# Optimization experiments

Measured on AMD Instinct MI355X. Metric: run time of the kernel, lower is better.

## Reference

```python
import jax, jax.numpy as jnp
import numpy as np
from jax import lax

B, S, D, H = 256, 1024, 64, 128


def setup_inputs() -> dict:
    key = jax.random.key(0)
    ks = jax.random.split(key, 11)
    s_in = 1.0 / np.sqrt(H)  # torch RNNCell/Linear init scale (uniform bound); normal scale ok for testing
    return {
        "inputs": jax.random.normal(ks[0], (B, S, D), jnp.float32),
        "Wih_fw": jax.random.normal(ks[1], (H, D), jnp.float32) * s_in,
        "Whh_fw": jax.random.normal(ks[2], (H, H), jnp.float32) * s_in,
        "bih_fw": jax.random.normal(ks[3], (H,), jnp.float32) * s_in,
        "bhh_fw": jax.random.normal(ks[4], (H,), jnp.float32) * s_in,
        "Wih_bw": jax.random.normal(ks[5], (H, D), jnp.float32) * s_in,
        "Whh_bw": jax.random.normal(ks[6], (H, H), jnp.float32) * s_in,
        "bih_bw": jax.random.normal(ks[7], (H,), jnp.float32) * s_in,
        "bhh_bw": jax.random.normal(ks[8], (H,), jnp.float32) * s_in,
        "fc_W": jax.random.normal(ks[9], (1, 2 * H), jnp.float32) * (1.0 / np.sqrt(2 * H)),
        "fc_b": jnp.zeros((1,), jnp.float32),
    }


def _run_dir(inputs, Wih, Whh, bih, bhh, reverse):
    # Precompute input projection for all timesteps: [B,S,H]
    xp = jnp.einsum('bsd,hd->bsh', inputs, Wih) + bih + bhh
    WhhT = Whh.T

    def step(h, x_t):  # x_t: [B,H]
        h_new = jnp.tanh(x_t + h @ WhhT)
        return h_new, h_new

    h0 = jnp.zeros((inputs.shape[0], Whh.shape[0]), inputs.dtype)
    # scan over time; reverse=True processes t = S-1..0 and emits outputs in
    # original time order, matching torch's output_bw[::-1] stacking.
    _, ys = lax.scan(step, h0, jnp.swapaxes(xp, 0, 1), reverse=reverse)
    return jnp.swapaxes(ys, 0, 1)  # [B,S,H]


def reference(inputs, Wih_fw, Whh_fw, bih_fw, bhh_fw,
              Wih_bw, Whh_bw, bih_bw, bhh_bw, fc_W, fc_b):
    out_fw = _run_dir(inputs, Wih_fw, Whh_fw, bih_fw, bhh_fw, reverse=False)
    out_bw = _run_dir(inputs, Wih_bw, Whh_bw, bih_bw, bhh_bw, reverse=True)
    outputs = jnp.concatenate([out_fw, out_bw], axis=2)  # [B,S,2H]
    outputs = outputs @ fc_W.T + fc_b  # [B,S,1]
    return jnp.squeeze(outputs, -1)  # [B,S]
```

## Files before the change

kernel.cpp:

```cpp
#include <hip/hip_runtime.h>

namespace {

constexpr int kS = 1024;
constexpr int kD = 64;
constexpr int kH = 128;

typedef __attribute__((ext_vector_type(2))) _Float16 half2v;
typedef __attribute__((ext_vector_type(4))) float f32x4;
typedef __attribute__((ext_vector_type(8))) _Float16 half8;

__device__ __forceinline__ float fdot2(unsigned w, unsigned h, float acc) {
#if __has_builtin(__builtin_amdgcn_fdot2)
  return __builtin_amdgcn_fdot2(__builtin_bit_cast(half2v, w),
                                __builtin_bit_cast(half2v, h), acc, false);
#else
  float d;
  asm("v_dot2_f32_f16 %0, %1, %2, %3" : "=v"(d) : "v"(w), "v"(h), "v"(acc));
  return d;
#endif
}

__device__ __forceinline__ unsigned pk16(float a, float b) {
  half2v h;
  h.x = (_Float16)a;
  h.y = (_Float16)b;
  return __builtin_bit_cast(unsigned, h);
}

__device__ __forceinline__ float fast_tanh(float x) {
  x = fminf(fmaxf(x, -15.f), 15.f);
  float e = __expf(2.f * x);
  return (e - 1.f) * __builtin_amdgcn_rcpf(e + 1.f);
}

#if __has_builtin(__builtin_amdgcn_mov_dpp)
__device__ __forceinline__ float lane_xor1(float v) {
  return __int_as_float(__builtin_amdgcn_mov_dpp(__float_as_int(v), 0xB1, 0xF, 0xF, true));
}
#else
__device__ __forceinline__ float lane_xor1(float v) {
  return __int_as_float(__builtin_amdgcn_ds_swizzle(__float_as_int(v), 0x041F));
}
#endif

__device__ __forceinline__ void stage_chunk(const char* g, unsigned* lds, int L) {
#pragma unroll
  for (int k = 0; k < 8; ++k) {
    __builtin_amdgcn_global_load_lds(
        (const __attribute__((address_space(1))) void*)(g + k * 1024 + L * 16),
        (__attribute__((address_space(3))) void*)(lds + k * 256), 16, 0, 0);
  }
}


__global__ __launch_bounds__(256, 2) void xproj_kernel(
    const float* __restrict__ inputs,
    const float* __restrict__ Wih_fw, const float* __restrict__ bih_fw,
    const float* __restrict__ bhh_fw,
    const float* __restrict__ Wih_bw, const float* __restrict__ bih_bw,
    const float* __restrict__ bhh_bw,
    _Float16* __restrict__ xp) {
  __shared__ _Float16 Wl[256 * 80];
  __shared__ _Float16 xl[128 * 80];
  __shared__ float biasl[256];

  const int tid = threadIdx.x;
  const int b = blockIdx.x;
  const int w = tid >> 6;
  const int lane = tid & 63;
  const int n16 = lane & 15;
  const int q = lane >> 4;

  {
    const int jd = tid;
    const float* src = (jd < kH) ? (Wih_fw + jd * kD) : (Wih_bw + (jd - kH) * kD);
    const float4* s4 = (const float4*)src;
#pragma unroll
    for (int k = 0; k < 8; ++k) {
      float4 a = s4[2 * k], c = s4[2 * k + 1];
      half8 h;
      h[0] = (_Float16)a.x; h[1] = (_Float16)a.y; h[2] = (_Float16)a.z; h[3] = (_Float16)a.w;
      h[4] = (_Float16)c.x; h[5] = (_Float16)c.y; h[6] = (_Float16)c.z; h[7] = (_Float16)c.w;
      *(half8*)&Wl[jd * 80 + k * 8] = h;
    }
    biasl[jd] = (jd < kH) ? (bih_fw[jd] + bhh_fw[jd])
                          : (bih_bw[jd - kH] + bhh_bw[jd - kH]);
  }

  for (int ch = 0; ch < 8; ++ch) {
    __syncthreads();
    {
      const int tl = tid >> 1, hf = tid & 1;
      const float4* s4 = (const float4*)(inputs +
          ((size_t)b * kS + ch * 128 + tl) * kD + hf * 32);
#pragma unroll
      for (int k = 0; k < 4; ++k) {
        float4 a = s4[2 * k], c = s4[2 * k + 1];
        half8 h;
        h[0] = (_Float16)a.x; h[1] = (_Float16)a.y; h[2] = (_Float16)a.z; h[3] = (_Float16)a.w;
        h[4] = (_Float16)c.x; h[5] = (_Float16)c.y; h[6] = (_Float16)c.z; h[7] = (_Float16)c.w;
        *(half8*)&xl[tl * 80 + hf * 32 + k * 8] = h;
      }
    }
    __syncthreads();

    half8 bf0[4], bf1[4];
    float bs[4];
#pragma unroll
    for (int nn = 0; nn < 4; ++nn) {
      const int jd = (w * 4 + nn) * 16 + n16;
      bf0[nn] = *(const half8*)&Wl[jd * 80 + q * 8];
      bf1[nn] = *(const half8*)&Wl[jd * 80 + q * 8 + 32];
      bs[nn] = biasl[jd];
    }

#pragma unroll 2
    for (int m = 0; m < 8; ++m) {
      const int trow = m * 16 + n16;
      const half8 a0 = *(const half8*)&xl[trow * 80 + q * 8];
      const half8 a1 = *(const half8*)&xl[trow * 80 + q * 8 + 32];
#pragma unroll
      for (int nn = 0; nn < 4; ++nn) {
        f32x4 acc = {0.f, 0.f, 0.f, 0.f};
        acc = __builtin_amdgcn_mfma_f32_16x16x32_f16(a0, bf0[nn], acc, 0, 0, 0);
        acc = __builtin_amdgcn_mfma_f32_16x16x32_f16(a1, bf1[nn], acc, 0, 0, 0);
        const int jd = (w * 4 + nn) * 16 + n16;
        const int dir = jd >> 7, j = jd & 127;
        const size_t slab = (size_t)(dir * 256 + b) * (kS * kH);
#pragma unroll
        for (int r = 0; r < 4; ++r) {
          const int t = ch * 128 + m * 16 + q * 4 + r;
          const int tt = dir ? (kS - 1 - t) : t;
          xp[slab + (size_t)(tt >> 5) * (32 * kH) + (tt & 31) * kH + j] =
              (_Float16)(acc[r] + bs[nn]);
        }
      }
    }
  }
}

__global__ __launch_bounds__(64, 1) void birnn_step_kernel(
    const _Float16* __restrict__ xp,
    const float* __restrict__ Whh_fw, const float* __restrict__ Whh_bw,
    const float* __restrict__ fcW, const float* __restrict__ fcb,
    float* __restrict__ out) {
  const int dir = blockIdx.x >> 8;
  const int b = blockIdx.x & 255;
  const int L = threadIdx.x;

  __shared__ unsigned jrn[32 * 68];
  __shared__ unsigned xbuf[2][2048];
  __shared__ unsigned fcwl[64];
  __shared__ float outbuf[kS];

  const float* __restrict__ Whh = dir ? Whh_bw : Whh_fw;

  unsigned w0[64], w1[64];
  {
    const float* r0 = Whh + (size_t)(2 * L) * kH;
    const float* r1 = Whh + (size_t)(2 * L + 1) * kH;
#pragma unroll
    for (int k = 0; k < 64; ++k) {
      w0[k] = pk16(r0[2 * k], r0[2 * k + 1]);
      w1[k] = pk16(r1[2 * k], r1[2 * k + 1]);
    }
  }
  fcwl[L] = pk16(fcW[dir * kH + 2 * L], fcW[dir * kH + 2 * L + 1]);
  jrn[31 * 68 + L] = 0;

  const char* slab = (const char*)(xp + (size_t)(dir * 256 + b) * (kS * kH));
  stage_chunk(slab, &xbuf[0][0], L);
  stage_chunk(slab + 8192, &xbuf[1][0], L);
  asm volatile("s_waitcnt vmcnt(0)" ::: "memory");

  for (int c = 0; c < 32; ++c) {
    const unsigned* xb = &xbuf[c & 1][0];

#pragma unroll 2
    for (int s = 0; s < 32; ++s) {
      const int prev = (s + 31) & 31;
      const uint4* hr = (const uint4*)&jrn[prev * 68];
      float a0 = 0.f, a1 = 0.f, a2 = 0.f, a3 = 0.f;
      float c0 = 0.f, c1 = 0.f, c2 = 0.f, c3 = 0.f;
#pragma unroll
      for (int g = 0; g < 16; ++g) {
        const uint4 hv = hr[g];
        a0 = fdot2(w0[4 * g + 0], hv.x, a0);
        c0 = fdot2(w1[4 * g + 0], hv.x, c0);
        a1 = fdot2(w0[4 * g + 1], hv.y, a1);
        c1 = fdot2(w1[4 * g + 1], hv.y, c1);
        a2 = fdot2(w0[4 * g + 2], hv.z, a2);
        c2 = fdot2(w1[4 * g + 2], hv.z, c2);
        a3 = fdot2(w0[4 * g + 3], hv.w, a3);
        c3 = fdot2(w1[4 * g + 3], hv.w, c3);
      }
      const half2v xh = __builtin_bit_cast(half2v, xb[s * 64 + L]);
      const float va = ((a0 + a1) + (a2 + a3)) + (float)xh.x;
      const float vb = ((c0 + c1) + (c2 + c3)) + (float)xh.y;
      jrn[s * 68 + L] = pk16(fast_tanh(va), fast_tanh(vb));
    }

    {
      const int tl = L >> 1, jh = L & 1;
      const uint4* rp = (const uint4*)&jrn[tl * 68 + jh * 32];
      const uint4* fp = (const uint4*)&fcwl[jh * 32];
      float acc = 0.f;
#pragma unroll
      for (int k = 0; k < 8; ++k) {
        const uint4 hv = rp[k];
        const uint4 fw = fp[k];
        acc = fdot2(fw.x, hv.x, acc);
        acc = fdot2(fw.y, hv.y, acc);
        acc = fdot2(fw.z, hv.z, acc);
        acc = fdot2(fw.w, hv.w, acc);
      }
      acc += lane_xor1(acc);
      if (jh == 0) outbuf[c * 32 + tl] = acc;
    }

    if (c < 30) {
      stage_chunk(slab + (size_t)(c + 2) * 8192, &xbuf[c & 1][0], L);
      asm volatile("s_waitcnt vmcnt(8)" ::: "memory");
    } else if (c == 30) {
      asm volatile("s_waitcnt vmcnt(0)" ::: "memory");
    }
  }

  const float fcb0 = (dir == 0) ? fcb[0] : 0.f;
#pragma unroll
  for (int k = 0; k < 16; ++k) {
    const int t = L + 64 * k;
    const int td = dir ? (kS - 1 - t) : t;
    atomicAdd(&out[(size_t)b * kS + td], outbuf[t] + fcb0);
  }
}

}

extern "C" void kernel_launch(void* const* d_in, const int* in_sizes, int n_in,
                              void* d_out, int out_size, void* d_ws, size_t ws_size,
                              hipStream_t stream) {
  (void)in_sizes; (void)n_in; (void)ws_size;
  const float* inputs = (const float*)d_in[0];
  const float* Wih_fw = (const float*)d_in[1];
  const float* Whh_fw = (const float*)d_in[2];
  const float* bih_fw = (const float*)d_in[3];
  const float* bhh_fw = (const float*)d_in[4];
  const float* Wih_bw = (const float*)d_in[5];
  const float* Whh_bw = (const float*)d_in[6];
  const float* bih_bw = (const float*)d_in[7];
  const float* bhh_bw = (const float*)d_in[8];
  const float* fc_W   = (const float*)d_in[9];
  const float* fc_b   = (const float*)d_in[10];
  float* out = (float*)d_out;
  _Float16* xpw = (_Float16*)d_ws;

  hipMemsetAsync(out, 0, (size_t)out_size * sizeof(float), stream);

  hipLaunchKernelGGL(xproj_kernel, dim3(256), dim3(256), 0, stream,
                     inputs, Wih_fw, bih_fw, bhh_fw, Wih_bw, bih_bw, bhh_bw, xpw);
  hipLaunchKernelGGL(birnn_step_kernel, dim3(512), dim3(64), 0, stream,
                     xpw, Whh_fw, Whh_bw, fc_W, fc_b, out);
}
```

Before: 570.6 us.

## Process two batch rows per wavefront to reuse register-resident Whh weights

Each 64-thread block now runs two independent batch sequences, so each register-held fp16 Whh value feeds two dot products per step. There are 256 blocks instead of 512, which gives each wave twice as many independent dot-product chains to hide latency. The tanh is simplified to 1-2/(e+1) without clamping, and prefetch of the next xp chunk is issued before the output projection. The trade-off is fewer waves across the GPU, so the serial 1024-step chain now carries twice the work per step.

```diff
diff --git a/kernel.cpp b/kernel.cpp
--- a/kernel.cpp
+++ b/kernel.cpp
@@ -29,9 +29,8 @@
 }
 
 __device__ __forceinline__ float fast_tanh(float x) {
-  x = fminf(fmaxf(x, -15.f), 15.f);
   float e = __expf(2.f * x);
-  return (e - 1.f) * __builtin_amdgcn_rcpf(e + 1.f);
+  return fmaf(-2.f, __builtin_amdgcn_rcpf(e + 1.f), 1.f);
 }
 
 #if __has_builtin(__builtin_amdgcn_mov_dpp)
@@ -145,83 +144,127 @@
     const float* __restrict__ Whh_fw, const float* __restrict__ Whh_bw,
     const float* __restrict__ fcW, const float* __restrict__ fcb,
     float* __restrict__ out) {
-  const int dir = blockIdx.x >> 8;
-  const int b = blockIdx.x & 255;
+  const int dir = blockIdx.x >> 7;
+  const int b0 = (blockIdx.x & 127) * 2;
   const int L = threadIdx.x;
 
-  __shared__ unsigned jrn[32 * 68];
-  __shared__ unsigned xbuf[2][2048];
+  __shared__ unsigned jrn[32 * 136];
+  __shared__ unsigned xbuf[2][2][2048];
   __shared__ unsigned fcwl[64];
-  __shared__ float outbuf[kS];
+  __shared__ float outbuf[2][kS];
 
   const float* __restrict__ Whh = dir ? Whh_bw : Whh_fw;
 
   unsigned w0[64], w1[64];
   {
-    const float* r0 = Whh + (size_t)(2 * L) * kH;
-    const float* r1 = Whh + (size_t)(2 * L + 1) * kH;
-#pragma unroll
-    for (int k = 0; k < 64; ++k) {
-      w0[k] = pk16(r0[2 * k], r0[2 * k + 1]);
-      w1[k] = pk16(r1[2 * k], r1[2 * k + 1]);
+    const float4* r0 = (const float4*)(Whh + (size_t)(2 * L) * kH);
+    const float4* r1 = (const float4*)(Whh + (size_t)(2 * L + 1) * kH);
+#pragma unroll
+    for (int k = 0; k < 32; ++k) {
+      const float4 v0 = r0[k], v1 = r1[k];
+      w0[2 * k + 0] = pk16(v0.x, v0.y);
+      w0[2 * k + 1] = pk16(v0.z, v0.w);
+      w1[2 * k + 0] = pk16(v1.x, v1.y);
+      w1[2 * k + 1] = pk16(v1.z, v1.w);
     }
   }
   fcwl[L] = pk16(fcW[dir * kH + 2 * L], fcW[dir * kH + 2 * L + 1]);
-  jrn[31 * 68 + L] = 0;
-
-  const char* slab = (const char*)(xp + (size_t)(dir * 256 + b) * (kS * kH));
-  stage_chunk(slab, &xbuf[0][0], L);
-  stage_chunk(slab + 8192, &xbuf[1][0], L);
+  jrn[31 * 136 + L] = 0;
+  jrn[31 * 136 + 68 + L] = 0;
+
+  const char* slabA = (const char*)(xp + (size_t)(dir * 256 + b0) * (kS * kH));
+  const char* slabB = (const char*)(xp + (size_t)(dir * 256 + b0 + 1) * (kS * kH));
+  stage_chunk(slabA, &xbuf[0][0][0], L);
+  stage_chunk(slabB, &xbuf[1][0][0], L);
+  stage_chunk(slabA + 8192, &xbuf[0][1][0], L);
+  stage_chunk(slabB + 8192, &xbuf[1][1][0], L);
   asm volatile("s_waitcnt vmcnt(0)" ::: "memory");
 
   for (int c = 0; c < 32; ++c) {
-    const unsigned* xb = &xbuf[c & 1][0];
-
-#pragma unroll 2
-    for (int s = 0; s < 32; ++s) {
-      const int prev = (s + 31) & 31;
-      const uint4* hr = (const uint4*)&jrn[prev * 68];
-      float a0 = 0.f, a1 = 0.f, a2 = 0.f, a3 = 0.f;
-      float c0 = 0.f, c1 = 0.f, c2 = 0.f, c3 = 0.f;
-#pragma unroll
-      for (int g = 0; g < 16; ++g) {
-        const uint4 hv = hr[g];
-        a0 = fdot2(w0[4 * g + 0], hv.x, a0);
-        c0 = fdot2(w1[4 * g + 0], hv.x, c0);
-        a1 = fdot2(w0[4 * g + 1], hv.y, a1);
-        c1 = fdot2(w1[4 * g + 1], hv.y, c1);
-        a2 = fdot2(w0[4 * g + 2], hv.z, a2);
-        c2 = fdot2(w1[4 * g + 2], hv.z, c2);
-        a3 = fdot2(w0[4 * g + 3], hv.w, a3);
-        c3 = fdot2(w1[4 * g + 3], hv.w, c3);
-      }
-      const half2v xh = __builtin_bit_cast(half2v, xb[s * 64 + L]);
-      const float va = ((a0 + a1) + (a2 + a3)) + (float)xh.x;
-      const float vb = ((c0 + c1) + (c2 + c3)) + (float)xh.y;
-      jrn[s * 68 + L] = pk16(fast_tanh(va), fast_tanh(vb));
+    const unsigned* xbA = &xbuf[0][c & 1][0];
+    const unsigned* xbB = &xbuf[1][c & 1][0];
+
+    for (int g = 0; g < 8; ++g) {
+      const uint4* bw = (const uint4*)&jrn[g * 4 * 136];
+      const uint4* br = (g == 0) ? (const uint4*)&jrn[31 * 136]
+                                 : (const uint4*)&jrn[(g * 4 - 1) * 136];
+#pragma unroll
+      for (int u = 0; u < 4; ++u) {
+        const int s = g * 4 + u;
+        const uint4* hA = (u == 0) ? br : (bw + (u - 1) * 34);
+        const uint4* hB = hA + 17;
+
+        float a0 = 0.f, a1 = 0.f, a2 = 0.f, a3 = 0.f;
+        float d0 = 0.f, d1 = 0.f, d2 = 0.f, d3 = 0.f;
+        float e0 = 0.f, e1 = 0.f, e2 = 0.f, e3 = 0.f;
+        float f0 = 0.f, f1 = 0.f, f2 = 0.f, f3 = 0.f;
+#pragma unroll
+        for (int g2 = 0; g2 < 16; ++g2) {
+          const uint4 vA = hA[g2];
+          const uint4 vB = hB[g2];
+          a0 = fdot2(w0[4 * g2 + 0], vA.x, a0);
+          d0 = fdot2(w1[4 * g2 + 0], vA.x, d0);
+          e0 = fdot2(w0[4 * g2 + 0], vB.x, e0);
+          f0 = fdot2(w1[4 * g2 + 0], vB.x, f0);
+          a1 = fdot2(w0[4 * g2 + 1], vA.y, a1);
+          d1 = fdot2(w1[4 * g2 + 1], vA.y, d1);
+          e1 = fdot2(w0[4 * g2 + 1], vB.y, e1);
+          f1 = fdot2(w1[4 * g2 + 1], vB.y, f1);
+          a2 = fdot2(w0[4 * g2 + 2], vA.z, a2);
+          d2 = fdot2(w1[4 * g2 + 2], vA.z, d2);
+          e2 = fdot2(w0[4 * g2 + 2], vB.z, e2);
+          f2 = fdot2(w1[4 * g2 + 2], vB.z, f2);
+          a3 = fdot2(w0[4 * g2 + 3], vA.w, a3);
+          d3 = fdot2(w1[4 * g2 + 3], vA.w, d3);
+          e3 = fdot2(w0[4 * g2 + 3], vB.w, e3);
+          f3 = fdot2(w1[4 * g2 + 3], vB.w, f3);
+        }
+        const half2v xA = __builtin_bit_cast(half2v, xbA[s * 64 + L]);
+        const half2v xB = __builtin_bit_cast(half2v, xbB[s * 64 + L]);
+        const float vAa = ((a0 + a1) + (a2 + a3)) + (float)xA.x;
+        const float vAd = ((d0 + d1) + (d2 + d3)) + (float)xA.y;
+        const float vBe = ((e0 + e1) + (e2 + e3)) + (float)xB.x;
+        const float vBf = ((f0 + f1) + (f2 + f3)) + (float)xB.y;
+        jrn[s * 136 + L] = pk16(fast_tanh(vAa), fast_tanh(vAd));
+        jrn[s * 136 + 68 + L] = pk16(fast_tanh(vBe), fast_tanh(vBf));
+      }
+    }
+
+    if (c < 30) {
+      stage_chunk(slabA + (size_t)(c + 2) * 8192, &xbuf[0][c & 1][0], L);
+      stage_chunk(slabB + (size_t)(c + 2) * 8192, &xbuf[1][c & 1][0], L);
     }
 
     {
       const int tl = L >> 1, jh = L & 1;
-      const uint4* rp = (const uint4*)&jrn[tl * 68 + jh * 32];
       const uint4* fp = (const uint4*)&fcwl[jh * 32];
-      float acc = 0.f;
+      const uint4* rpA = (const uint4*)&jrn[tl * 136 + jh * 32];
+      const uint4* rpB = (const uint4*)&jrn[tl * 136 + 68 + jh * 32];
+      float accA = 0.f, accB = 0.f;
 #pragma unroll
       for (int k = 0; k < 8; ++k) {
-        const uint4 hv = rp[k];
         const uint4 fw = fp[k];
-        acc = fdot2(fw.x, hv.x, acc);
-        acc = fdot2(fw.y, hv.y, acc);
-        acc = fdot2(fw.z, hv.z, acc);
-        acc = fdot2(fw.w, hv.w, acc);
-      }
-      acc += lane_xor1(acc);
-      if (jh == 0) outbuf[c * 32 + tl] = acc;
+        const uint4 hA = rpA[k];
+        const uint4 hB = rpB[k];
+        accA = fdot2(fw.x, hA.x, accA);
+        accB = fdot2(fw.x, hB.x, accB);
+        accA = fdot2(fw.y, hA.y, accA);
+        accB = fdot2(fw.y, hB.y, accB);
+        accA = fdot2(fw.z, hA.z, accA);
+        accB = fdot2(fw.z, hB.z, accB);
+        accA = fdot2(fw.w, hA.w, accA);
+        accB = fdot2(fw.w, hB.w, accB);
+      }
+      accA += lane_xor1(accA);
+      accB += lane_xor1(accB);
+      if (jh == 0) {
+        outbuf[0][c * 32 + tl] = accA;
+        outbuf[1][c * 32 + tl] = accB;
+      }
     }
 
     if (c < 30) {
-      stage_chunk(slab + (size_t)(c + 2) * 8192, &xbuf[c & 1][0], L);
-      asm volatile("s_waitcnt vmcnt(8)" ::: "memory");
+      asm volatile("s_waitcnt vmcnt(16)" ::: "memory");
     } else if (c == 30) {
       asm volatile("s_waitcnt vmcnt(0)" ::: "memory");
     }
@@ -232,7 +275,8 @@
   for (int k = 0; k < 16; ++k) {
     const int t = L + 64 * k;
     const int td = dir ? (kS - 1 - t) : t;
-    atomicAdd(&out[(size_t)b * kS + td], outbuf[t] + fcb0);
+    atomicAdd(&out[(size_t)b0 * kS + td], outbuf[0][t] + fcb0);
+    atomicAdd(&out[(size_t)(b0 + 1) * kS + td], outbuf[1][t] + fcb0);
   }
 }
 
@@ -260,6 +304,6 @@
 
   hipLaunchKernelGGL(xproj_kernel, dim3(256), dim3(256), 0, stream,
                      inputs, Wih_fw, bih_fw, bhh_fw, Wih_bw, bih_bw, bhh_bw, xpw);
-  hipLaunchKernelGGL(birnn_step_kernel, dim3(512), dim3(64), 0, stream,
+  hipLaunchKernelGGL(birnn_step_kernel, dim3(256), dim3(64), 0, stream,
                      xpw, Whh_fw, Whh_bw, fc_W, fc_b, out);
 }
```

Result: slower. 1.146 ms (+100.8%).

## Batch 16 sequences per block and run recurrence with MFMA instead of dot2

Applied to the files above, without the earlier changes.

The recurrent kernel now gives each block 16 batch rows of one direction and computes h @ Whh^T with 16x16x32 MFMA, holding Whh fragments in registers across two waves. The xproj output layout is interleaved so each timestep's 16 rows are contiguous. x tiles are double-buffered through registers into LDS, and the FC reduction is overlapped with later steps through a hidden-state ring. Only 32 blocks run, which uses few CUs and puts a barrier on every step, while tanh loses its input clamp.

```diff
diff --git a/kernel.cpp b/kernel.cpp
--- a/kernel.cpp
+++ b/kernel.cpp
@@ -29,28 +29,12 @@
 }
 
 __device__ __forceinline__ float fast_tanh(float x) {
-  x = fminf(fmaxf(x, -15.f), 15.f);
   float e = __expf(2.f * x);
-  return (e - 1.f) * __builtin_amdgcn_rcpf(e + 1.f);
-}
-
-#if __has_builtin(__builtin_amdgcn_mov_dpp)
-__device__ __forceinline__ float lane_xor1(float v) {
-  return __int_as_float(__builtin_amdgcn_mov_dpp(__float_as_int(v), 0xB1, 0xF, 0xF, true));
-}
-#else
-__device__ __forceinline__ float lane_xor1(float v) {
-  return __int_as_float(__builtin_amdgcn_ds_swizzle(__float_as_int(v), 0x041F));
-}
-#endif
-
-__device__ __forceinline__ void stage_chunk(const char* g, unsigned* lds, int L) {
-#pragma unroll
-  for (int k = 0; k < 8; ++k) {
-    __builtin_amdgcn_global_load_lds(
-        (const __attribute__((address_space(1))) void*)(g + k * 1024 + L * 16),
-        (__attribute__((address_space(3))) void*)(lds + k * 256), 16, 0, 0);
-  }
+  return fmaf(-2.f, __builtin_amdgcn_rcpf(e + 1.f), 1.f);
+}
+
+__device__ __forceinline__ void wave_barrier() {
+  asm volatile("s_waitcnt lgkmcnt(0)\n\ts_barrier" ::: "memory");
 }
 
 
@@ -88,6 +72,8 @@
                           : (bih_bw[jd - kH] + bhh_bw[jd - kH]);
   }
 
+  const int gb = b >> 4, ncol = b & 15;
+
   for (int ch = 0; ch < 8; ++ch) {
     __syncthreads();
     {
@@ -126,113 +112,174 @@
         acc = __builtin_amdgcn_mfma_f32_16x16x32_f16(a0, bf0[nn], acc, 0, 0, 0);
         acc = __builtin_amdgcn_mfma_f32_16x16x32_f16(a1, bf1[nn], acc, 0, 0, 0);
         const int jd = (w * 4 + nn) * 16 + n16;
-        const int dir = jd >> 7, j = jd & 127;
-        const size_t slab = (size_t)(dir * 256 + b) * (kS * kH);
+        const int dirx = jd >> 7, j = jd & 127;
+        const size_t slab = (size_t)(dirx * 16 + gb) * (kS * 2048);
 #pragma unroll
         for (int r = 0; r < 4; ++r) {
           const int t = ch * 128 + m * 16 + q * 4 + r;
-          const int tt = dir ? (kS - 1 - t) : t;
-          xp[slab + (size_t)(tt >> 5) * (32 * kH) + (tt & 31) * kH + j] =
-              (_Float16)(acc[r] + bs[nn]);
+          const int tt = dirx ? (kS - 1 - t) : t;
+          xp[slab + ((size_t)tt * 16 + ncol) * 128 + j] = (_Float16)(acc[r] + bs[nn]);
         }
       }
     }
   }
 }
 
-__global__ __launch_bounds__(64, 1) void birnn_step_kernel(
+__global__ __launch_bounds__(128, 1) void birnn_mfma_kernel(
     const _Float16* __restrict__ xp,
     const float* __restrict__ Whh_fw, const float* __restrict__ Whh_bw,
     const float* __restrict__ fcW, const float* __restrict__ fcb,
     float* __restrict__ out) {
-  const int dir = blockIdx.x >> 8;
-  const int b = blockIdx.x & 255;
-  const int L = threadIdx.x;
-
-  __shared__ unsigned jrn[32 * 68];
-  __shared__ unsigned xbuf[2][2048];
-  __shared__ unsigned fcwl[64];
-  __shared__ float outbuf[kS];
+  const int dir = blockIdx.x >> 4;
+  const int g = blockIdx.x & 15;
+  const int tid = threadIdx.x;
+  const int w = tid >> 6;
+  const int lane = tid & 63;
+  const int n = lane & 15;
+  const int q = lane >> 4;
+
+  __shared__ unsigned ring[8 * 1088];
+  __shared__ unsigned xbuf[2][4 * 1088];
+  __shared__ unsigned fcl[64];
 
   const float* __restrict__ Whh = dir ? Whh_bw : Whh_fw;
-
-  unsigned w0[64], w1[64];
-  {
-    const float* r0 = Whh + (size_t)(2 * L) * kH;
-    const float* r1 = Whh + (size_t)(2 * L + 1) * kH;
-#pragma unroll
-    for (int k = 0; k < 64; ++k) {
-      w0[k] = pk16(r0[2 * k], r0[2 * k + 1]);
-      w1[k] = pk16(r1[2 * k], r1[2 * k + 1]);
-    }
-  }
-  fcwl[L] = pk16(fcW[dir * kH + 2 * L], fcW[dir * kH + 2 * L + 1]);
-  jrn[31 * 68 + L] = 0;
-
-  const char* slab = (const char*)(xp + (size_t)(dir * 256 + b) * (kS * kH));
-  stage_chunk(slab, &xbuf[0][0], L);
-  stage_chunk(slab + 8192, &xbuf[1][0], L);
-  asm volatile("s_waitcnt vmcnt(0)" ::: "memory");
-
-  for (int c = 0; c < 32; ++c) {
-    const unsigned* xb = &xbuf[c & 1][0];
-
-#pragma unroll 2
-    for (int s = 0; s < 32; ++s) {
-      const int prev = (s + 31) & 31;
-      const uint4* hr = (const uint4*)&jrn[prev * 68];
-      float a0 = 0.f, a1 = 0.f, a2 = 0.f, a3 = 0.f;
-      float c0 = 0.f, c1 = 0.f, c2 = 0.f, c3 = 0.f;
-#pragma unroll
-      for (int g = 0; g < 16; ++g) {
-        const uint4 hv = hr[g];
-        a0 = fdot2(w0[4 * g + 0], hv.x, a0);
-        c0 = fdot2(w1[4 * g + 0], hv.x, c0);
-        a1 = fdot2(w0[4 * g + 1], hv.y, a1);
-        c1 = fdot2(w1[4 * g + 1], hv.y, c1);
-        a2 = fdot2(w0[4 * g + 2], hv.z, a2);
-        c2 = fdot2(w1[4 * g + 2], hv.z, c2);
-        a3 = fdot2(w0[4 * g + 3], hv.w, a3);
-        c3 = fdot2(w1[4 * g + 3], hv.w, c3);
-      }
-      const half2v xh = __builtin_bit_cast(half2v, xb[s * 64 + L]);
-      const float va = ((a0 + a1) + (a2 + a3)) + (float)xh.x;
-      const float vb = ((c0 + c1) + (c2 + c3)) + (float)xh.y;
-      jrn[s * 68 + L] = pk16(fast_tanh(va), fast_tanh(vb));
-    }
-
-    {
-      const int tl = L >> 1, jh = L & 1;
-      const uint4* rp = (const uint4*)&jrn[tl * 68 + jh * 32];
-      const uint4* fp = (const uint4*)&fcwl[jh * 32];
-      float acc = 0.f;
+  const float fcb0 = fcb[0];
+
+  half8 af[4][4];
+#pragma unroll
+  for (int ml = 0; ml < 4; ++ml)
+#pragma unroll
+    for (int kt = 0; kt < 4; ++kt) {
+      const float4* src =
+          (const float4*)(Whh + (size_t)(64 * w + 16 * ml + n) * kH + 32 * kt + 8 * q);
+      const float4 aa = src[0], bb = src[1];
+      half8 h;
+      h[0] = (_Float16)aa.x; h[1] = (_Float16)aa.y; h[2] = (_Float16)aa.z; h[3] = (_Float16)aa.w;
+      h[4] = (_Float16)bb.x; h[5] = (_Float16)bb.y; h[6] = (_Float16)bb.z; h[7] = (_Float16)bb.w;
+      af[ml][kt] = h;
+    }
+  if (tid < 64) fcl[tid] = pk16(fcW[dir * kH + 2 * tid], fcW[dir * kH + 2 * tid + 1]);
+#pragma unroll
+  for (int k = 0; k < 9; ++k) {
+    const int idx = tid + 128 * k;
+    if (idx < 1088) ring[7 * 1088 + idx] = 0;
+  }
+
+  const uint4* gx = (const uint4*)(xp + (size_t)(dir * 16 + g) * (kS * 2048));
+  uint4 rv[8];
+#pragma unroll
+  for (int k = 0; k < 8; ++k) rv[k] = gx[tid + 128 * k];
+#pragma unroll
+  for (int k = 0; k < 8; ++k) {
+    const int idx = tid + 128 * k;
+    const int t_loc = idx >> 8, rem = idx & 255, nn = rem >> 4, q4 = rem & 15;
+    *(uint4*)&xbuf[0][t_loc * 1088 + nn * 68 + 4 * q4] = rv[k];
+  }
+#pragma unroll
+  for (int k = 0; k < 8; ++k) rv[k] = gx[1024 + tid + 128 * k];
+  wave_barrier();
+
+  for (int c = 0; c < 256; ++c) {
+    const int cur = c & 1;
+    if (c < 255) {
 #pragma unroll
       for (int k = 0; k < 8; ++k) {
-        const uint4 hv = rp[k];
-        const uint4 fw = fp[k];
-        acc = fdot2(fw.x, hv.x, acc);
-        acc = fdot2(fw.y, hv.y, acc);
-        acc = fdot2(fw.z, hv.z, acc);
-        acc = fdot2(fw.w, hv.w, acc);
-      }
-      acc += lane_xor1(acc);
-      if (jh == 0) outbuf[c * 32 + tl] = acc;
-    }
-
-    if (c < 30) {
-      stage_chunk(slab + (size_t)(c + 2) * 8192, &xbuf[c & 1][0], L);
-      asm volatile("s_waitcnt vmcnt(8)" ::: "memory");
-    } else if (c == 30) {
-      asm volatile("s_waitcnt vmcnt(0)" ::: "memory");
-    }
-  }
-
-  const float fcb0 = (dir == 0) ? fcb[0] : 0.f;
-#pragma unroll
-  for (int k = 0; k < 16; ++k) {
-    const int t = L + 64 * k;
+        const int idx = tid + 128 * k;
+        const int t_loc = idx >> 8, rem = idx & 255, nn = rem >> 4, q4 = rem & 15;
+        *(uint4*)&xbuf[cur ^ 1][t_loc * 1088 + nn * 68 + 4 * q4] = rv[k];
+      }
+    }
+    if (c < 254) {
+#pragma unroll
+      for (int k = 0; k < 8; ++k) rv[k] = gx[(size_t)(c + 2) * 1024 + tid + 128 * k];
+    }
+    if (c > 0 && lane < 32) {
+      const int t_loc = 2 * w + (lane >> 4);
+      const int dn = lane & 15;
+      const int slot = 4 * (cur ^ 1) + t_loc;
+      const uint4* hr = (const uint4*)&ring[slot * 1088 + dn * 68];
+      const uint4* fp = (const uint4*)fcl;
+      float s = 0.f;
+#pragma unroll
+      for (int k2 = 0; k2 < 16; ++k2) {
+        const uint4 h = hr[k2], f = fp[k2];
+        s = fdot2(f.x, h.x, s);
+        s = fdot2(f.y, h.y, s);
+        s = fdot2(f.z, h.z, s);
+        s = fdot2(f.w, h.w, s);
+      }
+      const int t = (c - 1) * 4 + t_loc;
+      const int td = dir ? (kS - 1 - t) : t;
+      atomicAdd(&out[(size_t)(g * 16 + dn) * kS + td], s + (dir == 0 ? fcb0 : 0.f));
+    }
+
+#pragma unroll
+    for (int tl = 0; tl < 4; ++tl) {
+      const int wslot = cur * 4 + tl;
+      const int rslot = (wslot + 7) & 7;
+      const uint4* hrow = (const uint4*)&ring[rslot * 1088 + n * 68];
+      const half8 bf0 = __builtin_bit_cast(half8, hrow[q]);
+      const half8 bf1 = __builtin_bit_cast(half8, hrow[4 + q]);
+      const half8 bf2 = __builtin_bit_cast(half8, hrow[8 + q]);
+      const half8 bf3 = __builtin_bit_cast(half8, hrow[12 + q]);
+
+      const unsigned* xb = &xbuf[cur][tl * 1088 + n * 68];
+      f32x4 acc[4];
+#pragma unroll
+      for (int ml = 0; ml < 4; ++ml) {
+        const uint2 xv = *(const uint2*)&xb[8 * (4 * w + ml) + 2 * q];
+        const half2v x0 = __builtin_bit_cast(half2v, xv.x);
+        const half2v x1 = __builtin_bit_cast(half2v, xv.y);
+        f32x4 a;
+        a[0] = (float)x0.x; a[1] = (float)x0.y; a[2] = (float)x1.x; a[3] = (float)x1.y;
+        acc[ml] = a;
+      }
+#pragma unroll
+      for (int ml = 0; ml < 4; ++ml)
+        acc[ml] = __builtin_amdgcn_mfma_f32_16x16x32_f16(af[ml][0], bf0, acc[ml], 0, 0, 0);
+#pragma unroll
+      for (int ml = 0; ml < 4; ++ml)
+        acc[ml] = __builtin_amdgcn_mfma_f32_16x16x32_f16(af[ml][1], bf1, acc[ml], 0, 0, 0);
+#pragma unroll
+      for (int ml = 0; ml < 4; ++ml)
+        acc[ml] = __builtin_amdgcn_mfma_f32_16x16x32_f16(af[ml][2], bf2, acc[ml], 0, 0, 0);
+#pragma unroll
+      for (int ml = 0; ml < 4; ++ml)
+        acc[ml] = __builtin_amdgcn_mfma_f32_16x16x32_f16(af[ml][3], bf3, acc[ml], 0, 0, 0);
+
+#pragma unroll
+      for (int ml = 0; ml < 4; ++ml) {
+        const float t0 = fast_tanh(acc[ml][0]);
+        const float t1 = fast_tanh(acc[ml][1]);
+        const float t2 = fast_tanh(acc[ml][2]);
+        const float t3 = fast_tanh(acc[ml][3]);
+        uint2 o;
+        o.x = pk16(t0, t1);
+        o.y = pk16(t2, t3);
+        *(uint2*)&ring[wslot * 1088 + n * 68 + 8 * (4 * w + ml) + 2 * q] = o;
+      }
+      wave_barrier();
+    }
+  }
+
+  if (lane < 32) {
+    const int t_loc = 2 * w + (lane >> 4);
+    const int dn = lane & 15;
+    const int slot = 4 + t_loc;
+    const uint4* hr = (const uint4*)&ring[slot * 1088 + dn * 68];
+    const uint4* fp = (const uint4*)fcl;
+    float s = 0.f;
+#pragma unroll
+    for (int k2 = 0; k2 < 16; ++k2) {
+      const uint4 h = hr[k2], f = fp[k2];
+      s = fdot2(f.x, h.x, s);
+      s = fdot2(f.y, h.y, s);
+      s = fdot2(f.z, h.z, s);
+      s = fdot2(f.w, h.w, s);
+    }
+    const int t = 255 * 4 + t_loc;
     const int td = dir ? (kS - 1 - t) : t;
-    atomicAdd(&out[(size_t)b * kS + td], outbuf[t] + fcb0);
+    atomicAdd(&out[(size_t)(g * 16 + dn) * kS + td], s + (dir == 0 ? fcb0 : 0.f));
   }
 }
 
@@ -260,6 +307,6 @@
 
   hipLaunchKernelGGL(xproj_kernel, dim3(256), dim3(256), 0, stream,
                      inputs, Wih_fw, bih_fw, bhh_fw, Wih_bw, bih_bw, bhh_bw, xpw);
-  hipLaunchKernelGGL(birnn_step_kernel, dim3(512), dim3(64), 0, stream,
+  hipLaunchKernelGGL(birnn_mfma_kernel, dim3(32), dim3(128), 0, stream,
                      xpw, Whh_fw, Whh_bw, fc_W, fc_b, out);
 }
```

After: 1.057 ms. +85.2%, slower.
